# Kernel tuning notes

Hardware: AMD Instinct MI355X
Metric: run time of the kernel (lower is better)

## Reference

```python
import jax, jax.numpy as jnp
import numpy as np

F_IN, N_TREES, DEPTH, TREE_DIM, BATCH = 256, 512, 6, 3, 512


def entmax15_axis0(z):
    """Exact 1.5-entmax along axis 0 (sort-based algorithm from Peters et al. 2019)."""
    z = z / 2.0
    z = z - jnp.max(z, axis=0, keepdims=True)
    zs = -jnp.sort(-z, axis=0)                      # descending sort, [F, N]
    F = z.shape[0]
    rho = jnp.arange(1, F + 1, dtype=z.dtype)[:, None]
    mean = jnp.cumsum(zs, axis=0) / rho
    mean_sq = jnp.cumsum(zs * zs, axis=0) / rho
    ss = rho * (mean_sq - mean * mean)
    delta = (1.0 - ss) / rho
    tau = mean - jnp.sqrt(jnp.clip(delta, 0.0))
    support = (tau <= zs).astype(jnp.int32)
    k = jnp.sum(support, axis=0) - 1                # last valid index per column
    tau_star = jnp.take_along_axis(tau, k[None, :], axis=0)
    return jnp.square(jnp.clip(z - tau_star, 0.0))


def setup_inputs() -> dict:
    key = jax.random.key(0)
    k0, k1, k2, k3 = jax.random.split(key, 4)
    return {
        "input": jax.random.normal(k0, (BATCH, F_IN), jnp.float32),
        "feat_attention": jax.random.uniform(k1, (F_IN, N_TREES * DEPTH), jnp.float32),
        "feature_thresholds": jax.random.normal(k2, (N_TREES, DEPTH), jnp.float32) * 0.1,
        "log_temperatures": jnp.zeros((N_TREES, DEPTH), jnp.float32),
        "response": jax.random.normal(k3, (N_TREES, TREE_DIM, 2 ** DEPTH), jnp.float32),
    }


def reference(input, feat_attention, feature_thresholds, log_temperatures, response):
    T, D = feature_thresholds.shape
    F = feat_attention.shape[0]
    # sparse feature selection per (tree, depth)
    choice_weight = entmax15_axis0(feat_attention).reshape(F, T, D)
    feature_values = jnp.einsum('bi,ind->bnd', input, choice_weight)      # [B, T, D]
    # thresholding with learned temperature, bin_func == '05_01'
    tl = (feature_values - feature_thresholds) * jnp.exp(-log_temperatures)
    tl = jnp.stack([-tl, tl], axis=-1)                                    # [B, T, D, 2]
    bins = jnp.clip(0.5 * tl + 0.5, -0.5, 1.5)
    # binary codes of the 2^D leaves: [D, 2^D, 2]
    idx = jnp.arange(2 ** D)
    off = 2 ** jnp.arange(D)
    bc = ((idx[None, :] // off[:, None]) % 2).astype(bins.dtype)
    codes = jnp.stack([bc, 1.0 - bc], axis=-1)
    # depth-wise outer product into leaf weights
    bin_matches = jnp.einsum('btds,dcs->btdc', bins, codes)               # [B, T, D, 2^D]
    response_weights = jnp.prod(bin_matches, axis=-2)                     # [B, T, 2^D]
    out = jnp.einsum('bnd,ncd->bnc', response_weights, response)          # [B, T, C]
    return out.reshape(out.shape[0], -1)
```

## Files before the change

kernel.cpp:

```cpp
#include <hip/hip_runtime.h>
#include <math.h>

#define F_IN 256
#define NTREES 512
#define DEPTH 6
#define NCOLS (NTREES * DEPTH)
#define BATCH 512
#define OUTW (NTREES * 3)

typedef __attribute__((ext_vector_type(8))) short bf16x8;
typedef __attribute__((ext_vector_type(4))) float f32x4;
typedef __attribute__((ext_vector_type(4))) unsigned short u16x4;
typedef __attribute__((ext_vector_type(8))) unsigned short u16x8;

__device__ __forceinline__ unsigned short f2bf(float x) {
    unsigned u = __float_as_uint(x);
    return (unsigned short)((u + 0x7FFFu + ((u >> 16) & 1u)) >> 16);
}
__device__ __forceinline__ void split2(float x, unsigned short& h, unsigned short& l) {
    h = f2bf(x);
    l = f2bf(x - __uint_as_float((unsigned)h << 16));
}

__global__ __launch_bounds__(256) void k_entmax(const float* __restrict__ att,
                                                const float* __restrict__ inp,
                                                unsigned short* __restrict__ cwT_hi,
                                                unsigned short* __restrict__ cwT_lo,
                                                unsigned short* __restrict__ in_hi,
                                                unsigned short* __restrict__ in_lo) {
    const int tid = threadIdx.x;

    if (blockIdx.x >= NCOLS / 16) {
        const int cb = blockIdx.x - NCOLS / 16;
        const float4* src = (const float4*)inp;
#pragma unroll
        for (int it = 0; it < 16; ++it) {
            int idx = cb * 4096 + it * 256 + tid;
            float4 v = src[idx];
            u16x4 h, l;
            unsigned short th, tl;
            split2(v.x, th, tl); h.x = th; l.x = tl;
            split2(v.y, th, tl); h.y = th; l.y = tl;
            split2(v.z, th, tl); h.z = th; l.z = tl;
            split2(v.w, th, tl); h.w = th; l.w = tl;
            *(u16x4*)&in_hi[idx * 4] = h;
            *(u16x4*)&in_lo[idx * 4] = l;
        }
        return;
    }

    const int n0 = blockIdx.x * 16;
    const int lane = tid & 63;
    const int w = tid >> 6;
    __shared__ float s_z[16][260];

    const int cld = tid & 15;
#pragma unroll
    for (int it = 0; it < 16; ++it) {
        int f = (tid >> 4) + it * 16;
        s_z[cld][f] = att[f * NCOLS + n0 + cld];
    }
    __syncthreads();

    float4 z[4];
    float m[4], tau[4];
#pragma unroll
    for (int c = 0; c < 4; ++c) {
        float4 v = *(const float4*)&s_z[w * 4 + c][4 * lane];
        z[c] = make_float4(v.x * 0.5f, v.y * 0.5f, v.z * 0.5f, v.w * 0.5f);
        m[c] = fmaxf(fmaxf(z[c].x, z[c].y), fmaxf(z[c].z, z[c].w));
    }
#pragma unroll
    for (int off = 32; off >= 1; off >>= 1)
#pragma unroll
        for (int c = 0; c < 4; ++c)
            m[c] = fmaxf(m[c], __shfl_xor(m[c], off));
#pragma unroll
    for (int c = 0; c < 4; ++c) {
        z[c].x -= m[c]; z[c].y -= m[c]; z[c].z -= m[c]; z[c].w -= m[c];
        tau[c] = -1.0f;
    }

    for (int iter = 0; iter < 14; ++iter) {
        float S1[4], S2[4];
#pragma unroll
        for (int c = 0; c < 4; ++c) {
            float d0 = fmaxf(z[c].x - tau[c], 0.f);
            float d1 = fmaxf(z[c].y - tau[c], 0.f);
            float d2 = fmaxf(z[c].z - tau[c], 0.f);
            float d3 = fmaxf(z[c].w - tau[c], 0.f);
            S1[c] = (d0 + d1) + (d2 + d3);
            S2[c] = fmaf(d0, d0, fmaf(d1, d1, fmaf(d2, d2, d3 * d3)));
        }
#pragma unroll
        for (int off = 32; off >= 1; off >>= 1)
#pragma unroll
            for (int c = 0; c < 4; ++c) {
                S1[c] += __shfl_xor(S1[c], off);
                S2[c] += __shfl_xor(S2[c], off);
            }
        bool done = true;
#pragma unroll
        for (int c = 0; c < 4; ++c) {
            tau[c] += (S2[c] - 1.f) / (2.f * S1[c]);
            done = done && (fabsf(S2[c] - 1.f) < 4e-6f);
        }
        if (done) break;
    }

#pragma unroll
    for (int c = 0; c < 4; ++c) {
        float4 pv;
        float v0 = fmaxf(z[c].x - tau[c], 0.f);
        float v1 = fmaxf(z[c].y - tau[c], 0.f);
        float v2 = fmaxf(z[c].z - tau[c], 0.f);
        float v3 = fmaxf(z[c].w - tau[c], 0.f);
        pv.x = v0 * v0; pv.y = v1 * v1; pv.z = v2 * v2; pv.w = v3 * v3;
        *(float4*)&s_z[w * 4 + c][4 * lane] = pv;
    }
    __syncthreads();
    const int nl = tid >> 4;
    const int f0 = (tid & 15) * 16;
#pragma unroll
    for (int j = 0; j < 2; ++j) {
        u16x8 hv, lv;
#pragma unroll
        for (int e = 0; e < 8; ++e) {
            unsigned short h, l;
            split2(s_z[nl][f0 + j * 8 + e], h, l);
            hv[e] = h; lv[e] = l;
        }
        *(u16x8*)&cwT_hi[(n0 + nl) * F_IN + f0 + j * 8] = hv;
        *(u16x8*)&cwT_lo[(n0 + nl) * F_IN + f0 + j * 8] = lv;
    }
}

__global__ __launch_bounds__(256) void k_fused(const unsigned short* __restrict__ Ah,
                                               const unsigned short* __restrict__ Al,
                                               const unsigned short* __restrict__ Bh,
                                               const unsigned short* __restrict__ Bl,
                                               const float* __restrict__ thr,
                                               const float* __restrict__ ltemp,
                                               const float* __restrict__ resp,
                                               float* __restrict__ out) {
    const int tb  = blockIdx.x;
    const int b0  = blockIdx.y * 128;
    const int t0g = tb * 8;
    const int n0g = tb * 48;
    const int tid = threadIdx.x;
    const int wave = tid >> 6, lane = tid & 63;
    const int quad = lane >> 4, lr = lane & 15;

    __shared__ float sFV[48][132];
    __shared__ float sR[8 * 192];
    __shared__ float sTH[48], sET[48];
    __shared__ float sO[128][25];

    for (int i = tid; i < 8 * 192; i += 256) sR[i] = resp[t0g * 192 + i];
    if (tid < 48) {
        sTH[tid] = thr[n0g + tid];
        sET[tid] = expf(-ltemp[n0g + tid]);
    }

    const int bw = b0 + wave * 32;
    const unsigned short* pah = Ah + (n0g + lr) * F_IN + quad * 8;
    const unsigned short* pal = Al + (n0g + lr) * F_IN + quad * 8;
    const unsigned short* pbh = Bh + (bw + lr) * F_IN + quad * 8;
    const unsigned short* pbl = Bl + (bw + lr) * F_IN + quad * 8;

    f32x4 acc[3][2];
#pragma unroll
    for (int i = 0; i < 3; ++i)
#pragma unroll
        for (int j = 0; j < 2; ++j)
            acc[i][j] = (f32x4){0.f, 0.f, 0.f, 0.f};

#pragma unroll
    for (int k0 = 0; k0 < F_IN; k0 += 32) {
        bf16x8 ah[3], al[3], bh[2], bl[2];
#pragma unroll
        for (int i = 0; i < 3; ++i) {
            ah[i] = *(const bf16x8*)(pah + i * 16 * F_IN + k0);
            al[i] = *(const bf16x8*)(pal + i * 16 * F_IN + k0);
        }
#pragma unroll
        for (int j = 0; j < 2; ++j) {
            bh[j] = *(const bf16x8*)(pbh + j * 16 * F_IN + k0);
            bl[j] = *(const bf16x8*)(pbl + j * 16 * F_IN + k0);
        }
#pragma unroll
        for (int i = 0; i < 3; ++i)
#pragma unroll
            for (int j = 0; j < 2; ++j) {
                acc[i][j] = __builtin_amdgcn_mfma_f32_16x16x32_bf16(ah[i], bh[j], acc[i][j], 0, 0, 0);
                acc[i][j] = __builtin_amdgcn_mfma_f32_16x16x32_bf16(ah[i], bl[j], acc[i][j], 0, 0, 0);
                acc[i][j] = __builtin_amdgcn_mfma_f32_16x16x32_bf16(al[i], bh[j], acc[i][j], 0, 0, 0);
            }
    }
#pragma unroll
    for (int i = 0; i < 3; ++i)
#pragma unroll
        for (int j = 0; j < 2; ++j)
#pragma unroll
            for (int r = 0; r < 4; ++r)
                sFV[16 * i + quad * 4 + r][wave * 32 + 16 * j + lr] = acc[i][j][r];
    __syncthreads();

#pragma unroll
    for (int p = 0; p < 4; ++p) {
        const int pi = p * 256 + tid;
        const int tl = pi >> 7;
        const int b  = pi & 127;
        float bpos[6], bneg[6];
#pragma unroll
        for (int d = 0; d < 6; ++d) {
            float fvv = sFV[tl * 6 + d][b];
            float tlv = (fvv - sTH[tl * 6 + d]) * sET[tl * 6 + d];
            float hp = 0.5f * tlv + 0.5f;
            float hn = 0.5f - 0.5f * tlv;
            bpos[d] = fminf(fmaxf(hp, -0.5f), 1.5f);
            bneg[d] = fminf(fmaxf(hn, -0.5f), 1.5f);
        }
        float pr[64];
        pr[0] = 1.f;
#pragma unroll
        for (int d = 0; d < 6; ++d) {
            int half = 1 << d;
#pragma unroll 32
            for (int i = half - 1; i >= 0; --i) {
                float v = pr[i];
                pr[i + half] = v * bneg[d];
                pr[i]        = v * bpos[d];
            }
        }
        float a0 = 0.f, a1 = 0.f, a2 = 0.f;
        const float* r = &sR[tl * 192];
#pragma unroll
        for (int c = 0; c < 64; ++c) {
            a0 = fmaf(pr[c], r[c], a0);
            a1 = fmaf(pr[c], r[64 + c], a1);
            a2 = fmaf(pr[c], r[128 + c], a2);
        }
        sO[b][tl * 3 + 0] = a0;
        sO[b][tl * 3 + 1] = a1;
        sO[b][tl * 3 + 2] = a2;
    }
    __syncthreads();
    for (int i = tid; i < 128 * 24; i += 256) {
        int row = i / 24, col = i % 24;
        out[(b0 + row) * OUTW + t0g * 3 + col] = sO[row][col];
    }
}

extern "C" void kernel_launch(void* const* d_in, const int* in_sizes, int n_in,
                              void* d_out, int out_size, void* d_ws, size_t ws_size,
                              hipStream_t stream) {
    const float* input = (const float*)d_in[0];
    const float* att   = (const float*)d_in[1];
    const float* thr   = (const float*)d_in[2];
    const float* ltemp = (const float*)d_in[3];
    const float* resp  = (const float*)d_in[4];
    float* out = (float*)d_out;

    unsigned short* cwT_hi = (unsigned short*)d_ws;
    unsigned short* cwT_lo = cwT_hi + NCOLS * F_IN;
    unsigned short* in_hi  = cwT_lo + NCOLS * F_IN;
    unsigned short* in_lo  = in_hi + BATCH * F_IN;

    hipLaunchKernelGGL(k_entmax, dim3(NCOLS / 16 + 8), dim3(256), 0, stream,
                       att, input, cwT_hi, cwT_lo, in_hi, in_lo);
    hipLaunchKernelGGL(k_fused, dim3(NTREES / 8, BATCH / 128), dim3(256), 0, stream,
                       cwT_hi, cwT_lo, in_hi, in_lo, thr, ltemp, resp, out);
}
```

Measured before the change: 91.83 us.

## Split entmax columns across 16-lane groups, fuse input bf16 split into GEMM

The entmax kernel now gives each 16-lane group its own column, so the max and Newton reductions need only four shuffle steps instead of six and each wave exits as soon as its four columns converge. The separate input hi/lo conversion blocks are removed, and the fused kernel instead loads fp32 input and splits it to bf16 in registers before the MFMAs. The fused kernel moves to 512 threads with one 16-row batch tile per wave. Response, threshold and temperature values are read straight from global memory through a wave-uniform pointer rather than staged in shared memory. This saves a workspace round trip and some shuffles, but each block now repeats the input conversion, and the per-leaf response reads may cost more than LDS reads did.

```diff
diff --git a/kernel.cpp b/kernel.cpp
--- a/kernel.cpp
+++ b/kernel.cpp
@@ -10,7 +10,6 @@
 
 typedef __attribute__((ext_vector_type(8))) short bf16x8;
 typedef __attribute__((ext_vector_type(4))) float f32x4;
-typedef __attribute__((ext_vector_type(4))) unsigned short u16x4;
 typedef __attribute__((ext_vector_type(8))) unsigned short u16x8;
 
 __device__ __forceinline__ unsigned short f2bf(float x) {
@@ -23,36 +22,16 @@
 }
 
 __global__ __launch_bounds__(256) void k_entmax(const float* __restrict__ att,
-                                                const float* __restrict__ inp,
                                                 unsigned short* __restrict__ cwT_hi,
-                                                unsigned short* __restrict__ cwT_lo,
-                                                unsigned short* __restrict__ in_hi,
-                                                unsigned short* __restrict__ in_lo) {
+                                                unsigned short* __restrict__ cwT_lo) {
     const int tid = threadIdx.x;
-
-    if (blockIdx.x >= NCOLS / 16) {
-        const int cb = blockIdx.x - NCOLS / 16;
-        const float4* src = (const float4*)inp;
-#pragma unroll
-        for (int it = 0; it < 16; ++it) {
-            int idx = cb * 4096 + it * 256 + tid;
-            float4 v = src[idx];
-            u16x4 h, l;
-            unsigned short th, tl;
-            split2(v.x, th, tl); h.x = th; l.x = tl;
-            split2(v.y, th, tl); h.y = th; l.y = tl;
-            split2(v.z, th, tl); h.z = th; l.z = tl;
-            split2(v.w, th, tl); h.w = th; l.w = tl;
-            *(u16x4*)&in_hi[idx * 4] = h;
-            *(u16x4*)&in_lo[idx * 4] = l;
-        }
-        return;
-    }
-
     const int n0 = blockIdx.x * 16;
     const int lane = tid & 63;
     const int w = tid >> 6;
-    __shared__ float s_z[16][260];
+    const int g = lane >> 4;
+    const int li = lane & 15;
+
+    __shared__ __align__(16) float s_z[16][260];
 
     const int cld = tid & 15;
 #pragma unroll
@@ -62,83 +41,78 @@
     }
     __syncthreads();
 
+    const int c = w * 4 + g;
     float4 z[4];
-    float m[4], tau[4];
-#pragma unroll
-    for (int c = 0; c < 4; ++c) {
-        float4 v = *(const float4*)&s_z[w * 4 + c][4 * lane];
-        z[c] = make_float4(v.x * 0.5f, v.y * 0.5f, v.z * 0.5f, v.w * 0.5f);
-        m[c] = fmaxf(fmaxf(z[c].x, z[c].y), fmaxf(z[c].z, z[c].w));
-    }
-#pragma unroll
-    for (int off = 32; off >= 1; off >>= 1)
-#pragma unroll
-        for (int c = 0; c < 4; ++c)
-            m[c] = fmaxf(m[c], __shfl_xor(m[c], off));
-#pragma unroll
-    for (int c = 0; c < 4; ++c) {
-        z[c].x -= m[c]; z[c].y -= m[c]; z[c].z -= m[c]; z[c].w -= m[c];
-        tau[c] = -1.0f;
-    }
-
+#pragma unroll
+    for (int j = 0; j < 4; ++j) {
+        float4 v = *(const float4*)&s_z[c][li * 16 + 4 * j];
+        z[j] = make_float4(v.x * 0.5f, v.y * 0.5f, v.z * 0.5f, v.w * 0.5f);
+    }
+    float m = fmaxf(fmaxf(fmaxf(z[0].x, z[0].y), fmaxf(z[0].z, z[0].w)),
+                    fmaxf(fmaxf(z[1].x, z[1].y), fmaxf(z[1].z, z[1].w)));
+    m = fmaxf(m, fmaxf(fmaxf(fmaxf(z[2].x, z[2].y), fmaxf(z[2].z, z[2].w)),
+                       fmaxf(fmaxf(z[3].x, z[3].y), fmaxf(z[3].z, z[3].w))));
+#pragma unroll
+    for (int off = 8; off >= 1; off >>= 1) m = fmaxf(m, __shfl_xor(m, off));
+#pragma unroll
+    for (int j = 0; j < 4; ++j) {
+        z[j].x -= m; z[j].y -= m; z[j].z -= m; z[j].w -= m;
+    }
+
+    float tau = -1.0f;
     for (int iter = 0; iter < 14; ++iter) {
-        float S1[4], S2[4];
-#pragma unroll
-        for (int c = 0; c < 4; ++c) {
-            float d0 = fmaxf(z[c].x - tau[c], 0.f);
-            float d1 = fmaxf(z[c].y - tau[c], 0.f);
-            float d2 = fmaxf(z[c].z - tau[c], 0.f);
-            float d3 = fmaxf(z[c].w - tau[c], 0.f);
-            S1[c] = (d0 + d1) + (d2 + d3);
-            S2[c] = fmaf(d0, d0, fmaf(d1, d1, fmaf(d2, d2, d3 * d3)));
-        }
-#pragma unroll
-        for (int off = 32; off >= 1; off >>= 1)
-#pragma unroll
-            for (int c = 0; c < 4; ++c) {
-                S1[c] += __shfl_xor(S1[c], off);
-                S2[c] += __shfl_xor(S2[c], off);
-            }
-        bool done = true;
-#pragma unroll
-        for (int c = 0; c < 4; ++c) {
-            tau[c] += (S2[c] - 1.f) / (2.f * S1[c]);
-            done = done && (fabsf(S2[c] - 1.f) < 4e-6f);
-        }
-        if (done) break;
-    }
-
-#pragma unroll
-    for (int c = 0; c < 4; ++c) {
+        float s1p[4], s2p[4];
+#pragma unroll
+        for (int j = 0; j < 4; ++j) {
+            float d0 = fmaxf(z[j].x - tau, 0.f);
+            float d1 = fmaxf(z[j].y - tau, 0.f);
+            float d2 = fmaxf(z[j].z - tau, 0.f);
+            float d3 = fmaxf(z[j].w - tau, 0.f);
+            s1p[j] = (d0 + d1) + (d2 + d3);
+            s2p[j] = fmaf(d0, d0, fmaf(d1, d1, fmaf(d2, d2, d3 * d3)));
+        }
+        float s1 = (s1p[0] + s1p[1]) + (s1p[2] + s1p[3]);
+        float s2 = (s2p[0] + s2p[1]) + (s2p[2] + s2p[3]);
+#pragma unroll
+        for (int off = 8; off >= 1; off >>= 1) {
+            s1 += __shfl_xor(s1, off);
+            s2 += __shfl_xor(s2, off);
+        }
+        tau += (s2 - 1.f) / (2.f * s1);
+        if (__all(fabsf(s2 - 1.f) < 4e-6f)) break;
+    }
+
+#pragma unroll
+    for (int j = 0; j < 4; ++j) {
         float4 pv;
-        float v0 = fmaxf(z[c].x - tau[c], 0.f);
-        float v1 = fmaxf(z[c].y - tau[c], 0.f);
-        float v2 = fmaxf(z[c].z - tau[c], 0.f);
-        float v3 = fmaxf(z[c].w - tau[c], 0.f);
+        float v0 = fmaxf(z[j].x - tau, 0.f);
+        float v1 = fmaxf(z[j].y - tau, 0.f);
+        float v2 = fmaxf(z[j].z - tau, 0.f);
+        float v3 = fmaxf(z[j].w - tau, 0.f);
         pv.x = v0 * v0; pv.y = v1 * v1; pv.z = v2 * v2; pv.w = v3 * v3;
-        *(float4*)&s_z[w * 4 + c][4 * lane] = pv;
-    }
-    __syncthreads();
+        *(float4*)&s_z[c][li * 16 + 4 * j] = pv;
+    }
+    __syncthreads();
+
     const int nl = tid >> 4;
     const int f0 = (tid & 15) * 16;
 #pragma unroll
-    for (int j = 0; j < 2; ++j) {
+    for (int jj = 0; jj < 2; ++jj) {
         u16x8 hv, lv;
 #pragma unroll
         for (int e = 0; e < 8; ++e) {
             unsigned short h, l;
-            split2(s_z[nl][f0 + j * 8 + e], h, l);
+            split2(s_z[nl][f0 + jj * 8 + e], h, l);
             hv[e] = h; lv[e] = l;
         }
-        *(u16x8*)&cwT_hi[(n0 + nl) * F_IN + f0 + j * 8] = hv;
-        *(u16x8*)&cwT_lo[(n0 + nl) * F_IN + f0 + j * 8] = lv;
-    }
-}
-
-__global__ __launch_bounds__(256) void k_fused(const unsigned short* __restrict__ Ah,
+        *(u16x8*)&cwT_hi[(n0 + nl) * F_IN + f0 + jj * 8] = hv;
+        *(u16x8*)&cwT_lo[(n0 + nl) * F_IN + f0 + jj * 8] = lv;
+    }
+}
+
+__global__ __launch_bounds__(512) void k_fused(const unsigned short* __restrict__ Ah,
                                                const unsigned short* __restrict__ Al,
-                                               const unsigned short* __restrict__ Bh,
-                                               const unsigned short* __restrict__ Bl,
+                                               const float* __restrict__ inp,
                                                const float* __restrict__ thr,
                                                const float* __restrict__ ltemp,
                                                const float* __restrict__ resp,
@@ -152,70 +126,63 @@
     const int quad = lane >> 4, lr = lane & 15;
 
     __shared__ float sFV[48][132];
-    __shared__ float sR[8 * 192];
-    __shared__ float sTH[48], sET[48];
     __shared__ float sO[128][25];
 
-    for (int i = tid; i < 8 * 192; i += 256) sR[i] = resp[t0g * 192 + i];
-    if (tid < 48) {
-        sTH[tid] = thr[n0g + tid];
-        sET[tid] = expf(-ltemp[n0g + tid]);
-    }
-
-    const int bw = b0 + wave * 32;
+    const int bw = b0 + wave * 16;
     const unsigned short* pah = Ah + (n0g + lr) * F_IN + quad * 8;
     const unsigned short* pal = Al + (n0g + lr) * F_IN + quad * 8;
-    const unsigned short* pbh = Bh + (bw + lr) * F_IN + quad * 8;
-    const unsigned short* pbl = Bl + (bw + lr) * F_IN + quad * 8;
-
-    f32x4 acc[3][2];
-#pragma unroll
-    for (int i = 0; i < 3; ++i)
-#pragma unroll
-        for (int j = 0; j < 2; ++j)
-            acc[i][j] = (f32x4){0.f, 0.f, 0.f, 0.f};
+    const float* pbf = inp + (bw + lr) * F_IN + quad * 8;
+
+    f32x4 acc[3];
+#pragma unroll
+    for (int i = 0; i < 3; ++i) acc[i] = (f32x4){0.f, 0.f, 0.f, 0.f};
 
 #pragma unroll
     for (int k0 = 0; k0 < F_IN; k0 += 32) {
-        bf16x8 ah[3], al[3], bh[2], bl[2];
+        bf16x8 ah[3], al[3], bh, bl;
 #pragma unroll
         for (int i = 0; i < 3; ++i) {
             ah[i] = *(const bf16x8*)(pah + i * 16 * F_IN + k0);
             al[i] = *(const bf16x8*)(pal + i * 16 * F_IN + k0);
         }
-#pragma unroll
-        for (int j = 0; j < 2; ++j) {
-            bh[j] = *(const bf16x8*)(pbh + j * 16 * F_IN + k0);
-            bl[j] = *(const bf16x8*)(pbl + j * 16 * F_IN + k0);
-        }
-#pragma unroll
-        for (int i = 0; i < 3; ++i)
-#pragma unroll
-            for (int j = 0; j < 2; ++j) {
-                acc[i][j] = __builtin_amdgcn_mfma_f32_16x16x32_bf16(ah[i], bh[j], acc[i][j], 0, 0, 0);
-                acc[i][j] = __builtin_amdgcn_mfma_f32_16x16x32_bf16(ah[i], bl[j], acc[i][j], 0, 0, 0);
-                acc[i][j] = __builtin_amdgcn_mfma_f32_16x16x32_bf16(al[i], bh[j], acc[i][j], 0, 0, 0);
-            }
+        float4 v0 = *(const float4*)(pbf + k0);
+        float4 v1 = *(const float4*)(pbf + k0 + 4);
+        float fb[8] = {v0.x, v0.y, v0.z, v0.w, v1.x, v1.y, v1.z, v1.w};
+#pragma unroll
+        for (int e = 0; e < 8; ++e) {
+            unsigned short hh, ll;
+            split2(fb[e], hh, ll);
+            bh[e] = (short)hh; bl[e] = (short)ll;
+        }
+#pragma unroll
+        for (int i = 0; i < 3; ++i) {
+            acc[i] = __builtin_amdgcn_mfma_f32_16x16x32_bf16(ah[i], bh, acc[i], 0, 0, 0);
+            acc[i] = __builtin_amdgcn_mfma_f32_16x16x32_bf16(ah[i], bl, acc[i], 0, 0, 0);
+            acc[i] = __builtin_amdgcn_mfma_f32_16x16x32_bf16(al[i], bh, acc[i], 0, 0, 0);
+        }
     }
 #pragma unroll
     for (int i = 0; i < 3; ++i)
 #pragma unroll
-        for (int j = 0; j < 2; ++j)
-#pragma unroll
-            for (int r = 0; r < 4; ++r)
-                sFV[16 * i + quad * 4 + r][wave * 32 + 16 * j + lr] = acc[i][j][r];
-    __syncthreads();
-
-#pragma unroll
-    for (int p = 0; p < 4; ++p) {
-        const int pi = p * 256 + tid;
+        for (int r = 0; r < 4; ++r)
+            sFV[16 * i + quad * 4 + r][wave * 16 + lr] = acc[i][r];
+    __syncthreads();
+
+#pragma unroll
+    for (int p = 0; p < 2; ++p) {
+        const int pi = p * 512 + tid;
         const int tl = pi >> 7;
         const int b  = pi & 127;
+        const int tls = __builtin_amdgcn_readfirstlane(tl);
+        const float* rp = resp + (size_t)(t0g + tls) * 192;
+        const float* tp = thr   + (t0g + tls) * 6;
+        const float* lp = ltemp + (t0g + tls) * 6;
+
         float bpos[6], bneg[6];
 #pragma unroll
         for (int d = 0; d < 6; ++d) {
-            float fvv = sFV[tl * 6 + d][b];
-            float tlv = (fvv - sTH[tl * 6 + d]) * sET[tl * 6 + d];
+            float fvv = sFV[tls * 6 + d][b];
+            float tlv = (fvv - tp[d]) * __expf(-lp[d]);
             float hp = 0.5f * tlv + 0.5f;
             float hn = 0.5f - 0.5f * tlv;
             bpos[d] = fminf(fmaxf(hp, -0.5f), 1.5f);
@@ -234,19 +201,18 @@
             }
         }
         float a0 = 0.f, a1 = 0.f, a2 = 0.f;
-        const float* r = &sR[tl * 192];
-#pragma unroll
-        for (int c = 0; c < 64; ++c) {
-            a0 = fmaf(pr[c], r[c], a0);
-            a1 = fmaf(pr[c], r[64 + c], a1);
-            a2 = fmaf(pr[c], r[128 + c], a2);
+#pragma unroll
+        for (int cc = 0; cc < 64; ++cc) {
+            a0 = fmaf(pr[cc], rp[cc], a0);
+            a1 = fmaf(pr[cc], rp[64 + cc], a1);
+            a2 = fmaf(pr[cc], rp[128 + cc], a2);
         }
         sO[b][tl * 3 + 0] = a0;
         sO[b][tl * 3 + 1] = a1;
         sO[b][tl * 3 + 2] = a2;
     }
     __syncthreads();
-    for (int i = tid; i < 128 * 24; i += 256) {
+    for (int i = tid; i < 128 * 24; i += 512) {
         int row = i / 24, col = i % 24;
         out[(b0 + row) * OUTW + t0g * 3 + col] = sO[row][col];
     }
@@ -264,11 +230,9 @@
 
     unsigned short* cwT_hi = (unsigned short*)d_ws;
     unsigned short* cwT_lo = cwT_hi + NCOLS * F_IN;
-    unsigned short* in_hi  = cwT_lo + NCOLS * F_IN;
-    unsigned short* in_lo  = in_hi + BATCH * F_IN;
-
-    hipLaunchKernelGGL(k_entmax, dim3(NCOLS / 16 + 8), dim3(256), 0, stream,
-                       att, input, cwT_hi, cwT_lo, in_hi, in_lo);
-    hipLaunchKernelGGL(k_fused, dim3(NTREES / 8, BATCH / 128), dim3(256), 0, stream,
-                       cwT_hi, cwT_lo, in_hi, in_lo, thr, ltemp, resp, out);
-}
+
+    hipLaunchKernelGGL(k_entmax, dim3(NCOLS / 16), dim3(256), 0, stream,
+                       att, cwT_hi, cwT_lo);
+    hipLaunchKernelGGL(k_fused, dim3(NTREES / 8, BATCH / 128), dim3(512), 0, stream,
+                       cwT_hi, cwT_lo, input, thr, ltemp, resp, out);
+}
```

Result: no change. 90.79 us (-1.1%).
